# Optimization experiments

Measured on AMD Instinct MI355X. Metric: run time of the kernel, lower is better.

The kernel has to match this reference:

```python
import jax, jax.numpy as jnp
import numpy as np

EPS = 1e-12  # matches F.normalize default eps


def _l2norm(x, axis):
    n = jnp.sqrt(jnp.sum(x * x, axis=axis, keepdims=True))
    return x / jnp.maximum(n, EPS)


def setup_inputs() -> dict:
    key = jax.random.key(0)
    k1, k2 = jax.random.split(key)
    B, G, D, K = 512, 100, 768, 100
    h = jax.random.normal(k1, (B, G, D), dtype=jnp.float32)
    duplicate_pooling = jax.random.normal(k2, (G, D, K), dtype=jnp.float32)
    out_extrap = jnp.zeros((B, G, K), dtype=jnp.float32)
    return {"h": h, "duplicate_pooling": duplicate_pooling, "out_extrap": out_extrap}


def reference(h, duplicate_pooling, out_extrap):
    # Per-group: L2-normalize h_i over feature dim, L2-normalize w_i over its
    # first (feature) dim, then matmul. Fused across the group dim G.
    h_n = _l2norm(h, axis=-1)                       # [B, G, D]
    w_n = _l2norm(duplicate_pooling, axis=1)        # [G, D, K], normalize over D (dim=0 of each w_i)
    out = jnp.einsum("bgd,gdk->bgk", h_n, w_n)     # [B, G, K]
    return out
```

## Files before the change

kernel.cpp:

```cpp
#include <hip/hip_runtime.h>
#include <stdint.h>


#define G_    100
#define D_    768
#define K_    100
#define B_    512
#define KP_   128
#define BM    64
#define BK    64
#define NT    7
#define NITER (D_ / BK)

typedef __attribute__((ext_vector_type(8))) short bf16x8;
typedef __attribute__((ext_vector_type(4))) float f32x4;

__device__ __forceinline__ short f2bf(float f) {
    uint32_t u = __builtin_bit_cast(uint32_t, f);
    u = (u + 0x7FFFu + ((u >> 16) & 1u)) >> 16;
    return (short)u;
}

__device__ __forceinline__ void gl_lds16(const void* g, void* l) {
    __builtin_amdgcn_global_load_lds(
        (const __attribute__((address_space(1))) uint32_t*)g,
        (__attribute__((address_space(3))) uint32_t*)l, 16, 0, 0);
}

__global__ __launch_bounds__(256) void wprep(const float* __restrict__ W,
                                             short* __restrict__ Wt,
                                             float* __restrict__ wpart) {
    int bid = blockIdx.x;
    int g = bid / 12, dc = bid % 12;
    int d0 = dc * 64;
    int t = threadIdx.x;
    __shared__ float tile[64][104];

    for (int s = t; s < 64 * 25; s += 256) {
        int d = s / 25, j = s % 25;
        const float4 v = *(const float4*)(W + ((size_t)(g * D_ + d0 + d)) * K_ + j * 4);
        tile[d][j * 4 + 0] = v.x; tile[d][j * 4 + 1] = v.y;
        tile[d][j * 4 + 2] = v.z; tile[d][j * 4 + 3] = v.w;
    }
    __syncthreads();

    int kp = t >> 1, h2 = t & 1;
    float ss = 0.f;
    short* dst = Wt + ((size_t)(g * KP_ + kp)) * D_ + d0 + h2 * 32;
    if (kp < K_) {
        #pragma unroll
        for (int c = 0; c < 4; ++c) {
            bf16x8 o;
            #pragma unroll
            for (int i = 0; i < 8; ++i) {
                float v = tile[h2 * 32 + c * 8 + i][kp];
                ss += v * v;
                o[i] = f2bf(v);
            }
            *(bf16x8*)(dst + c * 8) = o;
        }
    } else {
        bf16x8 z = {0, 0, 0, 0, 0, 0, 0, 0};
        #pragma unroll
        for (int c = 0; c < 4; ++c) *(bf16x8*)(dst + c * 8) = z;
    }
    ss += __shfl_xor(ss, 1);
    if (h2 == 0) wpart[(size_t)(g * 12 + dc) * KP_ + kp] = ss;
}

__global__ __launch_bounds__(256) void gemm(const float* __restrict__ h,
                                            const short* __restrict__ Wt,
                                            const float* __restrict__ wpart,
                                            float* __restrict__ out) {
    int bid = blockIdx.x;
    int g, mt;
    if (bid < 768) { g = (bid & 7) + 8 * (bid >> 6); mt = (bid >> 3) & 7; }
    else           { int l = bid - 768; g = 96 + (l & 3); mt = l >> 2; }
    int b0 = mt * BM;
    int t = threadIdx.x;
    int w = t >> 6, lane = t & 63;
    int r = lane & 15, hh = lane >> 4;

    __shared__ __align__(16) short Bs[2][KP_ * BK];
    __shared__ float invw[KP_];
    __shared__ float hss[BM];

    const short* wtg = Wt + (size_t)g * KP_ * D_;

    if (t < KP_) {
        float s2 = 0.f;
        #pragma unroll
        for (int c = 0; c < 12; ++c) s2 += wpart[(size_t)(g * 12 + c) * KP_ + t];
        invw[t] = 1.f / fmaxf(sqrtf(s2), 1e-12f);
    }

    const float* hp = h + ((size_t)((b0 + w * 16 + r) * G_ + g)) * D_ + hh * 8;

    auto stageB = [&](int kt, int p) {
        char* base = (char*)&Bs[p][0];
        #pragma unroll
        for (int i = 0; i < 4; ++i) {
            int c = w * 4 + i;
            int kp = c * 8 + (lane >> 3);
            int colb = (lane & 7) * 16;
            int scol = colb ^ ((kp & 7) << 4);
            const char* src = (const char*)(wtg + (size_t)kp * D_ + kt * BK) + scol;
            gl_lds16(src, base + c * 1024);
        }
    };

    f32x4 acc[NT];
    #pragma unroll
    for (int i = 0; i < NT; ++i) acc[i] = (f32x4){0.f, 0.f, 0.f, 0.f};
    float ss = 0.f;

    stageB(0, 0);
    float4 a00 = *(const float4*)(hp + 0);
    float4 a01 = *(const float4*)(hp + 4);
    float4 a10 = *(const float4*)(hp + 32);
    float4 a11 = *(const float4*)(hp + 36);

    for (int kt = 0; kt < NITER; ++kt) {
        int p = kt & 1;
        __syncthreads();

        float4 n00 = {0,0,0,0}, n01 = {0,0,0,0}, n10 = {0,0,0,0}, n11 = {0,0,0,0};
        if (kt + 1 < NITER) {
            stageB(kt + 1, p ^ 1);
            const float* np = hp + (kt + 1) * BK;
            n00 = *(const float4*)(np + 0);
            n01 = *(const float4*)(np + 4);
            n10 = *(const float4*)(np + 32);
            n11 = *(const float4*)(np + 36);
        }

        float av[16] = {a00.x, a00.y, a00.z, a00.w, a01.x, a01.y, a01.z, a01.w,
                        a10.x, a10.y, a10.z, a10.w, a11.x, a11.y, a11.z, a11.w};
        bf16x8 af0, af1;
        #pragma unroll
        for (int i = 0; i < 8; ++i) { ss += av[i] * av[i];         af0[i] = f2bf(av[i]); }
        #pragma unroll
        for (int i = 0; i < 8; ++i) { ss += av[8 + i] * av[8 + i]; af1[i] = f2bf(av[8 + i]); }

        const char* bb = (const char*)&Bs[p][0];
        int swz = (r & 7) << 4;
        #pragma unroll
        for (int nt = 0; nt < NT; ++nt) {
            int rowb = (nt * 16 + r) * 128;
            bf16x8 bv0 = *(const bf16x8*)(bb + rowb + ((hh * 16) ^ swz));
            bf16x8 bv1 = *(const bf16x8*)(bb + rowb + ((64 + hh * 16) ^ swz));
            acc[nt] = __builtin_amdgcn_mfma_f32_16x16x32_bf16(af0, bv0, acc[nt], 0, 0, 0);
            acc[nt] = __builtin_amdgcn_mfma_f32_16x16x32_bf16(af1, bv1, acc[nt], 0, 0, 0);
        }
        a00 = n00; a01 = n01; a10 = n10; a11 = n11;
    }

    ss += __shfl_xor(ss, 16);
    ss += __shfl_xor(ss, 32);
    if (hh == 0) hss[w * 16 + r] = ss;
    __syncthreads();

    int rbase = hh * 4;
    float ih[4];
    #pragma unroll
    for (int q = 0; q < 4; ++q) ih[q] = 1.f / fmaxf(sqrtf(hss[w * 16 + rbase + q]), 1e-12f);
    #pragma unroll
    for (int nt = 0; nt < NT; ++nt) {
        int n = nt * 16 + r;
        if (n < K_) {
            float iw = invw[n];
            #pragma unroll
            for (int q = 0; q < 4; ++q) {
                int b = b0 + w * 16 + rbase + q;
                out[((size_t)b * G_ + g) * K_ + n] = acc[nt][q] * iw * ih[q];
            }
        }
    }
}

extern "C" void kernel_launch(void* const* d_in, const int* in_sizes, int n_in,
                              void* d_out, int out_size, void* d_ws, size_t ws_size,
                              hipStream_t stream) {
    const float* h = (const float*)d_in[0];
    const float* W = (const float*)d_in[1];
    float* out = (float*)d_out;

    short* Wt    = (short*)d_ws;
    float* wpart = (float*)((char*)d_ws + (size_t)G_ * KP_ * D_ * 2);

    wprep<<<dim3(G_ * 12), dim3(256), 0, stream>>>(W, Wt, wpart);
    gemm <<<dim3(G_ * 8),  dim3(256), 0, stream>>>(h, Wt, wpart, out);
}
```

Baseline: 286.7 us.

## Triple-buffer GEMM loads with explicit vmcnt waits and deferred weight-norm reduction

```diff
diff --git a/kernel.cpp b/kernel.cpp
--- a/kernel.cpp
+++ b/kernel.cpp
@@ -6,14 +6,18 @@
 #define D_    768
 #define K_    100
 #define B_    512
-#define KP_   128
+#define KP    128
+#define NW    112
 #define BM    64
 #define BK    64
 #define NT    7
 #define NITER (D_ / BK)
+#define DEPTH 3
 
 typedef __attribute__((ext_vector_type(8))) short bf16x8;
 typedef __attribute__((ext_vector_type(4))) float f32x4;
+
+#define FENCE() do { asm volatile("" ::: "memory"); __builtin_amdgcn_sched_barrier(0); } while (0)
 
 __device__ __forceinline__ short f2bf(float f) {
     uint32_t u = __builtin_bit_cast(uint32_t, f);
@@ -45,27 +49,29 @@
     __syncthreads();
 
     int kp = t >> 1, h2 = t & 1;
-    float ss = 0.f;
-    short* dst = Wt + ((size_t)(g * KP_ + kp)) * D_ + d0 + h2 * 32;
-    if (kp < K_) {
-        #pragma unroll
-        for (int c = 0; c < 4; ++c) {
-            bf16x8 o;
+    if (kp < NW) {
+        float ss = 0.f;
+        short* dst = Wt + ((size_t)(g * KP + kp)) * D_ + d0 + h2 * 32;
+        if (kp < K_) {
             #pragma unroll
-            for (int i = 0; i < 8; ++i) {
-                float v = tile[h2 * 32 + c * 8 + i][kp];
-                ss += v * v;
-                o[i] = f2bf(v);
+            for (int c = 0; c < 4; ++c) {
+                bf16x8 o;
+                #pragma unroll
+                for (int i = 0; i < 8; ++i) {
+                    float v = tile[h2 * 32 + c * 8 + i][kp];
+                    ss += v * v;
+                    o[i] = f2bf(v);
+                }
+                *(bf16x8*)(dst + c * 8) = o;
             }
-            *(bf16x8*)(dst + c * 8) = o;
-        }
-    } else {
-        bf16x8 z = {0, 0, 0, 0, 0, 0, 0, 0};
-        #pragma unroll
-        for (int c = 0; c < 4; ++c) *(bf16x8*)(dst + c * 8) = z;
-    }
-    ss += __shfl_xor(ss, 1);
-    if (h2 == 0) wpart[(size_t)(g * 12 + dc) * KP_ + kp] = ss;
+        } else {
+            bf16x8 z = {0, 0, 0, 0, 0, 0, 0, 0};
+            #pragma unroll
+            for (int c = 0; c < 4; ++c) *(bf16x8*)(dst + c * 8) = z;
+        }
+        ss += __shfl_xor(ss, 1);
+        if (h2 == 0) wpart[(size_t)(g * 12 + dc) * NW + kp] = ss;
+    }
 }
 
 __global__ __launch_bounds__(256) void gemm(const float* __restrict__ h,
@@ -81,19 +87,11 @@
     int w = t >> 6, lane = t & 63;
     int r = lane & 15, hh = lane >> 4;
 
-    __shared__ __align__(16) short Bs[2][KP_ * BK];
-    __shared__ float invw[KP_];
+    __shared__ __align__(16) short Bs[DEPTH][KP * BK];
+    __shared__ float invw[NW];
     __shared__ float hss[BM];
 
-    const short* wtg = Wt + (size_t)g * KP_ * D_;
-
-    if (t < KP_) {
-        float s2 = 0.f;
-        #pragma unroll
-        for (int c = 0; c < 12; ++c) s2 += wpart[(size_t)(g * 12 + c) * KP_ + t];
-        invw[t] = 1.f / fmaxf(sqrtf(s2), 1e-12f);
-    }
-
+    const short* wtg = Wt + (size_t)g * KP * D_;
     const float* hp = h + ((size_t)((b0 + w * 16 + r) * G_ + g)) * D_ + hh * 8;
 
     auto stageB = [&](int kt, int p) {
@@ -109,40 +107,47 @@
         }
     };
 
+    struct AReg { float4 v0, v1, v2, v3; };
+    auto loadA = [&](int kt) {
+        const float* p = hp + kt * BK;
+        AReg a;
+        a.v0 = *(const float4*)(p + 0);
+        a.v1 = *(const float4*)(p + 4);
+        a.v2 = *(const float4*)(p + 32);
+        a.v3 = *(const float4*)(p + 36);
+        return a;
+    };
+
     f32x4 acc[NT];
     #pragma unroll
     for (int i = 0; i < NT; ++i) acc[i] = (f32x4){0.f, 0.f, 0.f, 0.f};
     float ss = 0.f;
 
-    stageB(0, 0);
-    float4 a00 = *(const float4*)(hp + 0);
-    float4 a01 = *(const float4*)(hp + 4);
-    float4 a10 = *(const float4*)(hp + 32);
-    float4 a11 = *(const float4*)(hp + 36);
-
+    stageB(0, 0); AReg q0 = loadA(0); FENCE();
+    stageB(1, 1); AReg q1 = loadA(1); FENCE();
+    stageB(2, 2); AReg q2 = loadA(2); FENCE();
+    AReg q3 = q2;
+
+    #pragma unroll
     for (int kt = 0; kt < NITER; ++kt) {
-        int p = kt & 1;
-        __syncthreads();
-
-        float4 n00 = {0,0,0,0}, n01 = {0,0,0,0}, n10 = {0,0,0,0}, n11 = {0,0,0,0};
-        if (kt + 1 < NITER) {
-            stageB(kt + 1, p ^ 1);
-            const float* np = hp + (kt + 1) * BK;
-            n00 = *(const float4*)(np + 0);
-            n01 = *(const float4*)(np + 4);
-            n10 = *(const float4*)(np + 32);
-            n11 = *(const float4*)(np + 36);
-        }
-
-        float av[16] = {a00.x, a00.y, a00.z, a00.w, a01.x, a01.y, a01.z, a01.w,
-                        a10.x, a10.y, a10.z, a10.w, a11.x, a11.y, a11.z, a11.w};
+        if (kt <= 9)       asm volatile("s_waitcnt vmcnt(16)" ::: "memory");
+        else if (kt == 10) asm volatile("s_waitcnt vmcnt(8)"  ::: "memory");
+        else               asm volatile("s_waitcnt vmcnt(0)"  ::: "memory");
+        __builtin_amdgcn_sched_barrier(0);
+        __builtin_amdgcn_s_barrier();
+        FENCE();
+
+        float av[16] = {q0.v0.x, q0.v0.y, q0.v0.z, q0.v0.w,
+                        q0.v1.x, q0.v1.y, q0.v1.z, q0.v1.w,
+                        q0.v2.x, q0.v2.y, q0.v2.z, q0.v2.w,
+                        q0.v3.x, q0.v3.y, q0.v3.z, q0.v3.w};
         bf16x8 af0, af1;
         #pragma unroll
         for (int i = 0; i < 8; ++i) { ss += av[i] * av[i];         af0[i] = f2bf(av[i]); }
         #pragma unroll
         for (int i = 0; i < 8; ++i) { ss += av[8 + i] * av[8 + i]; af1[i] = f2bf(av[8 + i]); }
 
-        const char* bb = (const char*)&Bs[p][0];
+        const char* bb = (const char*)&Bs[kt % DEPTH][0];
         int swz = (r & 7) << 4;
         #pragma unroll
         for (int nt = 0; nt < NT; ++nt) {
@@ -152,12 +157,28 @@
             acc[nt] = __builtin_amdgcn_mfma_f32_16x16x32_bf16(af0, bv0, acc[nt], 0, 0, 0);
             acc[nt] = __builtin_amdgcn_mfma_f32_16x16x32_bf16(af1, bv1, acc[nt], 0, 0, 0);
         }
-        a00 = n00; a01 = n01; a10 = n10; a11 = n11;
+
+        FENCE();
+        __builtin_amdgcn_s_barrier();
+        FENCE();
+        if (kt + DEPTH < NITER) {
+            stageB(kt + DEPTH, kt % DEPTH);
+            q3 = loadA(kt + DEPTH);
+        }
+        q0 = q1; q1 = q2; q2 = q3;
+        FENCE();
     }
 
     ss += __shfl_xor(ss, 16);
     ss += __shfl_xor(ss, 32);
     if (hh == 0) hss[w * 16 + r] = ss;
+
+    if (t < NW) {
+        float s2 = 0.f;
+        #pragma unroll
+        for (int c = 0; c < 12; ++c) s2 += wpart[(size_t)(g * 12 + c) * NW + t];
+        invw[t] = 1.f / fmaxf(sqrtf(s2), 1e-12f);
+    }
     __syncthreads();
 
     int rbase = hh * 4;
@@ -186,7 +207,7 @@
     float* out = (float*)d_out;
 
     short* Wt    = (short*)d_ws;
-    float* wpart = (float*)((char*)d_ws + (size_t)G_ * KP_ * D_ * 2);
+    float* wpart = (float*)((char*)d_ws + (size_t)G_ * KP * D_ * 2);
 
     wprep<<<dim3(G_ * 12), dim3(256), 0, stream>>>(W, Wt, wpart);
     gemm <<<dim3(G_ * 8),  dim3(256), 0, stream>>>(h, Wt, wpart, out);
```

Result: slower. 298.4 us (+4.1%).
